# Performance work log

Measured on AMD Instinct MI355X. Metric: run time of the kernel, lower is better.

## Reference

```python
import jax, jax.numpy as jnp
import numpy as np

B, S, E, H, FF = 4, 2048, 1024, 16, 4096
DK = E // H
EPS = 1e-5


def setup_inputs() -> dict:
    key = jax.random.key(0)
    ks = jax.random.split(key, 16)
    sc = 0.02
    return {
        "x": jax.random.normal(ks[0], (B, S, E), jnp.float32),
        "Wq": jax.random.normal(ks[1], (E, E), jnp.float32) * sc,
        "Wk": jax.random.normal(ks[2], (E, E), jnp.float32) * sc,
        "Wv": jax.random.normal(ks[3], (E, E), jnp.float32) * sc,
        "Wo": jax.random.normal(ks[4], (E, E), jnp.float32) * sc,
        "theta": jax.random.normal(ks[5], (DK,), jnp.float32),
        "Wcq": jax.random.normal(ks[6], (E, E), jnp.float32) * sc,
        "ln1_g": jnp.ones((E,), jnp.float32),
        "ln1_b": jnp.zeros((E,), jnp.float32),
        "W1": jax.random.normal(ks[7], (E, FF), jnp.float32) * sc,
        "b1": jnp.zeros((FF,), jnp.float32),
        "W2": jax.random.normal(ks[8], (FF, E), jnp.float32) * sc,
        "b2": jnp.zeros((E,), jnp.float32),
        "ln2_g": jnp.ones((E,), jnp.float32),
        "ln2_b": jnp.zeros((E,), jnp.float32),
    }


def _layernorm(x, g, b):
    mu = jnp.mean(x, axis=-1, keepdims=True)
    var = jnp.mean(jnp.square(x - mu), axis=-1, keepdims=True)
    return (x - mu) * jax.lax.rsqrt(var + EPS) * g + b


def reference(x, Wq, Wk, Wv, Wo, theta, Wcq, ln1_g, ln1_b, W1, b1, W2, b2, ln2_g, ln2_b):
    mix = 0.5
    # classical multi-head attention
    def heads(t):  # [B,S,E] -> [B,H,S,DK]
        return t.reshape(B, S, H, DK).transpose(0, 2, 1, 3)
    q = heads(x @ Wq)
    k = heads(x @ Wk)
    v = heads(x @ Wv)
    scores = jnp.einsum("bhqd,bhkd->bhqk", q, k) / jnp.sqrt(jnp.float32(DK))
    attn = jax.nn.softmax(scores, axis=-1)
    ctx = jnp.einsum("bhqk,bhkd->bhqd", attn, v)
    ctx = ctx.transpose(0, 2, 1, 3).reshape(B, S, E)
    classical = ctx @ Wo
    # quantum heads: RX(x)RX(theta)|0>, <Z> = cos(x + theta), same theta shared per head
    qh = jnp.cos(x.reshape(B, S, H, DK) + theta)  # broadcast over wires
    quantum = qh.reshape(B, S, E) @ Wcq
    attn_out = mix * classical + (1.0 - mix) * quantum
    x1 = _layernorm(x + attn_out, ln1_g, ln1_b)
    ffn = jax.nn.relu(x1 @ W1 + b1) @ W2 + b2
    return _layernorm(x1 + ffn, ln2_g, ln2_b)
```

## Files before the change

kernel.cpp:

```cpp
#include <hip/hip_runtime.h>
#include <hip/hip_bf16.h>

typedef __bf16 bf16_t;
typedef bf16_t bf16x8 __attribute__((ext_vector_type(8)));
typedef bf16_t bf16x4v __attribute__((ext_vector_type(4)));
typedef float f32x4 __attribute__((ext_vector_type(4)));
typedef unsigned u32x4 __attribute__((ext_vector_type(4)));

static constexpr int EE = 1024;
static constexpr int SS = 2048;
static constexpr int DK = 64;
static constexpr float QSCALE = 0.125f * 1.44269504f;

__device__ __forceinline__ void gload_lds16(const void* g, void* l) {
  __builtin_amdgcn_global_load_lds(
      (__attribute__((address_space(1))) void*)g,
      (__attribute__((address_space(3))) void*)l, 16, 0, 0);
}

__device__ __forceinline__ f32x4 mfma16(bf16x8 a, bf16x8 b, f32x4 c) {
  return __builtin_amdgcn_mfma_f32_16x16x32_bf16(a, b, c, 0, 0, 0);
}

template<int OFF>
__device__ __forceinline__ bf16x4v tr8(unsigned va) {
  bf16x4v d;
  asm volatile("ds_read_b64_tr_b16 %0, %1 offset:%c2"
               : "=v"(d) : "v"(va), "i"(OFF));
  return d;
}

__global__ void __launch_bounds__(256) prep_x_kernel(
    const float* __restrict__ x, const float* __restrict__ theta,
    bf16_t* __restrict__ xbf, bf16_t* __restrict__ A2)
{
  const long t = (long)blockIdx.x * 256 + threadIdx.x;
  const long e0 = t * 8;
  const int col = (int)(e0 & (EE - 1));
  const long row = e0 >> 10;
  const float4 v0 = *(const float4*)&x[e0];
  const float4 v1 = *(const float4*)&x[e0 + 4];
  float xs[8] = {v0.x, v0.y, v0.z, v0.w, v1.x, v1.y, v1.z, v1.w};
  const int d0 = col & (DK - 1);
  bf16x8 xb, qb;
#pragma unroll
  for (int j = 0; j < 8; ++j) {
    xb[j] = (bf16_t)xs[j];
    qb[j] = (bf16_t)__cosf(xs[j] + theta[d0 + j]);
  }
  *(bf16x8*)&xbf[e0] = xb;
  *(bf16x8*)&A2[row * 2048 + EE + col] = qb;
}

__global__ void __launch_bounds__(256) transpose_all_kernel(
    const float* __restrict__ Wq, const float* __restrict__ Wk,
    const float* __restrict__ Wv, const float* __restrict__ Wo,
    const float* __restrict__ Wcq, const float* __restrict__ W1,
    const float* __restrict__ W2,
    bf16_t* __restrict__ BtQKV, bf16_t* __restrict__ Bt2,
    bf16_t* __restrict__ BtW1, bf16_t* __restrict__ BtW2)
{
  const int bid = blockIdx.x;
  const float* src; bf16_t* dst; int N; long dstride, dcol0; int bx, by;
  if (bid < 5120) {
    const int seg = bid >> 10, r = bid & 1023;
    bx = r & 31; by = r >> 5; N = 1024;
    if      (seg == 0) { src = Wq;  dst = BtQKV;               dstride = 1024; dcol0 = 0; }
    else if (seg == 1) { src = Wk;  dst = BtQKV + 1024 * 1024; dstride = 1024; dcol0 = 0; }
    else if (seg == 2) { src = Wv;  dst = BtQKV + 2048 * 1024; dstride = 1024; dcol0 = 0; }
    else if (seg == 3) { src = Wo;  dst = Bt2;                 dstride = 2048; dcol0 = 0; }
    else               { src = Wcq; dst = Bt2;                 dstride = 2048; dcol0 = 1024; }
  } else if (bid < 9216) {
    const int r = bid - 5120;
    src = W1; dst = BtW1; N = 4096; dstride = 1024; dcol0 = 0;
    bx = r & 127; by = r >> 7;
  } else {
    const int r = bid - 9216;
    src = W2; dst = BtW2; N = 1024; dstride = 4096; dcol0 = 0;
    bx = r & 31; by = r >> 5;
  }
  __shared__ float tile[32][33];
  const int tx = threadIdx.x, ty = threadIdx.y;
  const long n0 = (long)bx * 32, k0 = (long)by * 32;
#pragma unroll
  for (int j = 0; j < 4; ++j)
    tile[ty + j * 8][tx] = src[(k0 + ty + j * 8) * N + n0 + tx];
  __syncthreads();
#pragma unroll
  for (int j = 0; j < 4; ++j)
    dst[(n0 + ty + j * 8) * dstride + dcol0 + k0 + tx] = (bf16_t)tile[tx][ty + j * 8];
}

template<int MODE>
__global__ void __launch_bounds__(512, 4) gemm128(
    const bf16_t* __restrict__ A, const bf16_t* __restrict__ Bt,
    void* __restrict__ C, int M, int N, int K,
    const float* __restrict__ aux1, const bf16_t* __restrict__ aux2)
{
  __shared__ bf16_t As[3][256 * 32];
  __shared__ bf16_t Bs[3][128 * 32];
  const int tid = threadIdx.x;
  const int lane = tid & 63, wid = tid >> 6;
  const int wr = wid >> 1, wc = wid & 1;
  const int lr = lane & 15, lk = lane >> 4;
  const int gx = gridDim.x;
  const int nwg = gx * gridDim.y;
  const int bid = blockIdx.y * gx + blockIdx.x;
  const int swz = (bid & 7) * (nwg >> 3) + (bid >> 3);
  const long m0 = (long)(swz / gx) * 256;
  const long n0 = (long)(swz % gx) * 128;

  const int rql = lane >> 2;
  const int sl  = lane & 3;
  const int rA0 = wid * 32 + rql, rA1 = wid * 32 + 16 + rql;
  const bf16_t* sA0 = &A [(m0 + rA0) * K + 8 * (sl ^ ((rA0 >> 1) & 3))];
  const bf16_t* sA1 = &A [(m0 + rA1) * K + 8 * (sl ^ ((rA1 >> 1) & 3))];
  const int rB0 = wid * 16 + rql;
  const bf16_t* sB0 = &Bt[(n0 + rB0) * K + 8 * (sl ^ ((rB0 >> 1) & 3))];
  const int loA = wid * 1024;
  const int loB = wid * 512;

  f32x4 acc[4][4] = {};
  const int NKT = K / 32;

  auto stage = [&](int t) {
    const int s = t % 3;
    gload_lds16(sA0 + (long)t * 32, &As[s][loA]);
    gload_lds16(sA1 + (long)t * 32, &As[s][loA + 512]);
    gload_lds16(sB0 + (long)t * 32, &Bs[s][loB]);
  };

  stage(0); stage(1);
  asm volatile("s_waitcnt vmcnt(3)" ::: "memory");
  __builtin_amdgcn_s_barrier();

  for (int t = 0; t < NKT; ++t) {
    const int s = t % 3;
    bf16x8 bfr[4], af1[2], af2[2];
#pragma unroll
    for (int nb = 0; nb < 4; ++nb) {
      const int rw = wc * 64 + nb * 16 + lr;
      bfr[nb] = *(const bf16x8*)&Bs[s][rw * 32 + (lk ^ ((rw >> 1) & 3)) * 8];
    }
#pragma unroll
    for (int mb = 0; mb < 2; ++mb) {
      const int rw = wr * 64 + mb * 16 + lr;
      af1[mb] = *(const bf16x8*)&As[s][rw * 32 + (lk ^ ((rw >> 1) & 3)) * 8];
    }
    __builtin_amdgcn_sched_barrier(0);
#pragma unroll
    for (int mb = 0; mb < 2; ++mb) {
      const int rw = wr * 64 + 32 + mb * 16 + lr;
      af2[mb] = *(const bf16x8*)&As[s][rw * 32 + (lk ^ ((rw >> 1) & 3)) * 8];
    }
    if (t + 2 < NKT) stage(t + 2);
    asm volatile("s_waitcnt lgkmcnt(2)" ::: "memory");
    __builtin_amdgcn_sched_barrier(0);
    __builtin_amdgcn_s_setprio(1);
#pragma unroll
    for (int mb = 0; mb < 2; ++mb)
#pragma unroll
      for (int nb = 0; nb < 4; ++nb)
        acc[mb][nb] = mfma16(af1[mb], bfr[nb], acc[mb][nb]);
    __builtin_amdgcn_s_setprio(0);
    asm volatile("s_waitcnt lgkmcnt(0)" ::: "memory");
    __builtin_amdgcn_sched_barrier(0);
    __builtin_amdgcn_s_setprio(1);
#pragma unroll
    for (int mb = 0; mb < 2; ++mb)
#pragma unroll
      for (int nb = 0; nb < 4; ++nb)
        acc[2 + mb][nb] = mfma16(af2[mb], bfr[nb], acc[2 + mb][nb]);
    __builtin_amdgcn_s_setprio(0);
    if (t + 2 < NKT)      { asm volatile("s_waitcnt vmcnt(3)" ::: "memory"); }
    else if (t + 1 < NKT) { asm volatile("s_waitcnt vmcnt(0)" ::: "memory"); }
    __builtin_amdgcn_s_barrier();
  }

#pragma unroll
  for (int mb = 0; mb < 4; ++mb)
#pragma unroll
    for (int nb = 0; nb < 4; ++nb)
#pragma unroll
      for (int i = 0; i < 4; ++i) {
        const long r = m0 + wr * 64 + mb * 16 + lk * 4 + i;
        const long cc = n0 + wc * 64 + nb * 16 + lr;
        float v = acc[mb][nb][i];
        if constexpr (MODE == 0) {
          if (cc < 1024) v *= QSCALE;
          ((bf16_t*)C)[r * N + cc] = (bf16_t)v;
        } else if constexpr (MODE == 1) {
          ((bf16_t*)C)[r * N + cc] = (bf16_t)(0.5f * v + (float)aux2[r * N + cc]);
        } else if constexpr (MODE == 2) {
          ((bf16_t*)C)[r * N + cc] = (bf16_t)fmaxf(v + aux1[cc], 0.0f);
        } else {
          ((bf16_t*)C)[r * N + cc] = (bf16_t)(v + aux1[cc] + (float)aux2[r * N + cc]);
        }
      }
}

__global__ void __launch_bounds__(256, 2) attn_kernel(
    const bf16_t* __restrict__ QKV, bf16_t* __restrict__ Ctx)
{
  __shared__ bf16_t Ks[2][64 * 64];
  __shared__ bf16_t Vt[2][64 * 64];
  const int tid = threadIdx.x;
  const int lane = tid & 63, w = tid >> 6;
  const int lr = lane & 15, lk = lane >> 4;
  const int bh = blockIdx.x, b = bh >> 4, h = bh & 15;
  const long rowbase = (long)b * SS;
  const int q0 = blockIdx.y * 128;
  const int qcol = h * 64, kcol = EE + h * 64, vcol = 2 * EE + h * 64;
  constexpr int NT = SS / 64;

  bf16x8 qf[2][2];
#pragma unroll
  for (int mb = 0; mb < 2; ++mb)
#pragma unroll
    for (int ks = 0; ks < 2; ++ks)
      qf[mb][ks] = *(const bf16x8*)&QKV[
          (rowbase + q0 + w * 32 + mb * 16 + lr) * 3072 + qcol + ks * 32 + lk * 8];

  const int ksl = ((lane & 7) ^ ((lane >> 3) & 7)) * 8;
  const bf16_t* sK0 = &QKV[(rowbase + (2 * w + 0) * 8 + (lane >> 3)) * 3072 + kcol + ksl];
  const bf16_t* sK1 = &QKV[(rowbase + (2 * w + 1) * 8 + (lane >> 3)) * 3072 + kcol + ksl];
  const int vk = 4 * (lane >> 3) + ((lane >> 1) & 3);
  const int vd = 16 * w + 8 * (lane & 1);
  const bf16_t* sV0 = &QKV[(rowbase + vk) * 3072 + vcol + vd];
  const bf16_t* sV1 = &QKV[(rowbase + 32 + vk) * 3072 + vcol + vd];

  auto stage = [&](int t) {
    const int buf = t & 1;
    const long off = (long)t * 64 * 3072;
    gload_lds16(sK0 + off, &Ks[buf][(2 * w + 0) * 512]);
    gload_lds16(sK1 + off, &Ks[buf][(2 * w + 1) * 512]);
    gload_lds16(sV0 + off, &Vt[buf][(2 * w + 0) * 512]);
    gload_lds16(sV1 + off, &Vt[buf][(2 * w + 1) * 512]);
  };

  const unsigned vtr_base =
      (unsigned)(uintptr_t)(__attribute__((address_space(3))) void*)&Vt[0][0]
      + 2u * (unsigned)(lr + lk * 64);

  f32x4 oacc[2][4] = {};
  float lsum[2] = {0.0f, 0.0f};

  stage(0);

  for (int t = 0; t < NT; ++t) {
    const int buf = t & 1;
    __syncthreads();
    if (t + 1 < NT) stage(t + 1);

    bf16x8 kf[4][2];
#pragma unroll
    for (int nb = 0; nb < 4; ++nb)
#pragma unroll
      for (int ks = 0; ks < 2; ++ks)
        kf[nb][ks] = *(const bf16x8*)&Ks[buf][
            (nb * 16 + lr) * 64 + ((ks * 4 + lk) ^ (lr & 7)) * 8];
    __builtin_amdgcn_sched_barrier(0);

    const unsigned va = vtr_base + (unsigned)buf * 8192u;
    bf16x4v vlo[4][2], vhi[4][2];
    vlo[0][0] = tr8<   0>(va);  vhi[0][0] = tr8< 512>(va);
    vlo[0][1] = tr8<1024>(va);  vhi[0][1] = tr8<1536>(va);
    vlo[1][0] = tr8<2048>(va);  vhi[1][0] = tr8<2560>(va);
    vlo[1][1] = tr8<3072>(va);  vhi[1][1] = tr8<3584>(va);
    vlo[2][0] = tr8<4096>(va);  vhi[2][0] = tr8<4608>(va);
    vlo[2][1] = tr8<5120>(va);  vhi[2][1] = tr8<5632>(va);
    vlo[3][0] = tr8<6144>(va);  vhi[3][0] = tr8<6656>(va);
    vlo[3][1] = tr8<7168>(va);  vhi[3][1] = tr8<7680>(va);

    asm volatile("s_waitcnt lgkmcnt(15)" ::: "memory");
    __builtin_amdgcn_sched_barrier(0);

    f32x4 sacc[2][4] = {};
    __builtin_amdgcn_s_setprio(1);
#pragma unroll
    for (int mb = 0; mb < 2; ++mb)
#pragma unroll
      for (int nb = 0; nb < 4; ++nb)
#pragma unroll
        for (int ks = 0; ks < 2; ++ks)
          sacc[mb][nb] = mfma16(kf[nb][ks], qf[mb][ks], sacc[mb][nb]);
    __builtin_amdgcn_s_setprio(0);

    bf16x8 pfm[2][2];
#pragma unroll
    for (int mb = 0; mb < 2; ++mb) {
      float psum = 0.0f;
      u32x4 pk[2];
#pragma unroll
      for (int nb = 0; nb < 4; ++nb)
#pragma unroll
        for (int p = 0; p < 2; ++p) {
          const float a = __builtin_amdgcn_exp2f(sacc[mb][nb][2 * p]);
          const float bb = __builtin_amdgcn_exp2f(sacc[mb][nb][2 * p + 1]);
          psum += a + bb;
          unsigned pr;
          asm("v_cvt_pk_bf16_f32 %0, %1, %2" : "=v"(pr) : "v"(a), "v"(bb));
          pk[nb >> 1][(nb & 1) * 2 + p] = pr;
        }
      lsum[mb] += psum;
      pfm[mb][0] = __builtin_bit_cast(bf16x8, pk[0]);
      pfm[mb][1] = __builtin_bit_cast(bf16x8, pk[1]);
    }

    asm volatile("s_waitcnt lgkmcnt(0)" ::: "memory");
    __builtin_amdgcn_sched_barrier(0);
    bf16x8 vf[4][2];
#pragma unroll
    for (int nb = 0; nb < 4; ++nb)
#pragma unroll
      for (int ks = 0; ks < 2; ++ks)
        vf[nb][ks] = __builtin_shufflevector(
            vlo[nb][ks], vhi[nb][ks], 0, 1, 2, 3, 4, 5, 6, 7);
    __builtin_amdgcn_s_setprio(1);
#pragma unroll
    for (int mb = 0; mb < 2; ++mb)
#pragma unroll
      for (int nb = 0; nb < 4; ++nb)
#pragma unroll
        for (int ks = 0; ks < 2; ++ks)
          oacc[mb][nb] = mfma16(pfm[mb][ks], vf[nb][ks], oacc[mb][nb]);
    __builtin_amdgcn_s_setprio(0);
  }

#pragma unroll
  for (int mb = 0; mb < 2; ++mb) {
    float l = lsum[mb];
    l += __shfl_xor(l, 16);
    l += __shfl_xor(l, 32);
    float li[4];
#pragma unroll
    for (int i = 0; i < 4; ++i) li[i] = 1.0f / __shfl(l, lk * 4 + i);
#pragma unroll
    for (int nb = 0; nb < 4; ++nb)
#pragma unroll
      for (int i = 0; i < 4; ++i) {
        const long r = rowbase + q0 + w * 32 + mb * 16 + lk * 4 + i;
        Ctx[r * 2048 + h * 64 + nb * 16 + lr] = (bf16_t)(oacc[mb][nb][i] * li[i]);
      }
  }
}

__device__ __forceinline__ void ln_reduce4(const float4& v, int tid,
                                           float& mu, float& rs) {
  float s = v.x + v.y + v.z + v.w;
  float ss = v.x * v.x + v.y * v.y + v.z * v.z + v.w * v.w;
#pragma unroll
  for (int off = 1; off < 64; off <<= 1) {
    s += __shfl_xor(s, off);
    ss += __shfl_xor(ss, off);
  }
  __shared__ float wsum[4], wsq[4];
  if ((tid & 63) == 0) { wsum[tid >> 6] = s; wsq[tid >> 6] = ss; }
  __syncthreads();
  s = wsum[0] + wsum[1] + wsum[2] + wsum[3];
  ss = wsq[0] + wsq[1] + wsq[2] + wsq[3];
  mu = s * (1.0f / EE);
  rs = rsqrtf(ss * (1.0f / EE) - mu * mu + 1e-5f);
}

__global__ void __launch_bounds__(256) ln_bf16_kernel(
    const bf16_t* __restrict__ pre, const float* __restrict__ g,
    const float* __restrict__ bt, bf16_t* __restrict__ out)
{
  const int r = blockIdx.x, tid = threadIdx.x;
  const long base = (long)r * EE + tid * 4;
  const bf16x4v pv = *(const bf16x4v*)&pre[base];
  float4 v = make_float4((float)pv[0], (float)pv[1], (float)pv[2], (float)pv[3]);
  float mu, rs;
  ln_reduce4(v, tid, mu, rs);
  const float4 gv = *(const float4*)&g[tid * 4];
  const float4 bv = *(const float4*)&bt[tid * 4];
  bf16x4v o;
  o[0] = (bf16_t)((v.x - mu) * rs * gv.x + bv.x);
  o[1] = (bf16_t)((v.y - mu) * rs * gv.y + bv.y);
  o[2] = (bf16_t)((v.z - mu) * rs * gv.z + bv.z);
  o[3] = (bf16_t)((v.w - mu) * rs * gv.w + bv.w);
  *(bf16x4v*)&out[base] = o;
}

__global__ void __launch_bounds__(256) ln_f32_kernel(
    const bf16_t* __restrict__ pre, const float* __restrict__ g,
    const float* __restrict__ bt, float* __restrict__ out)
{
  const int r = blockIdx.x, tid = threadIdx.x;
  const long base = (long)r * EE + tid * 4;
  const bf16x4v pv = *(const bf16x4v*)&pre[base];
  float4 v = make_float4((float)pv[0], (float)pv[1], (float)pv[2], (float)pv[3]);
  float mu, rs;
  ln_reduce4(v, tid, mu, rs);
  const float4 gv = *(const float4*)&g[tid * 4];
  const float4 bv = *(const float4*)&bt[tid * 4];
  float4 o;
  o.x = (v.x - mu) * rs * gv.x + bv.x;
  o.y = (v.y - mu) * rs * gv.y + bv.y;
  o.z = (v.z - mu) * rs * gv.z + bv.z;
  o.w = (v.w - mu) * rs * gv.w + bv.w;
  *(float4*)&out[base] = o;
}

extern "C" void kernel_launch(void* const* d_in, const int* in_sizes, int n_in,
                              void* d_out, int out_size, void* d_ws, size_t ws_size,
                              hipStream_t stream)
{
  (void)in_sizes; (void)n_in; (void)out_size; (void)ws_size;
  const float* x     = (const float*)d_in[0];
  const float* Wq    = (const float*)d_in[1];
  const float* Wk    = (const float*)d_in[2];
  const float* Wv    = (const float*)d_in[3];
  const float* Wo    = (const float*)d_in[4];
  const float* theta = (const float*)d_in[5];
  const float* Wcq   = (const float*)d_in[6];
  const float* ln1g  = (const float*)d_in[7];
  const float* ln1b  = (const float*)d_in[8];
  const float* W1    = (const float*)d_in[9];
  const float* b1    = (const float*)d_in[10];
  const float* W2    = (const float*)d_in[11];
  const float* b2    = (const float*)d_in[12];
  const float* ln2g  = (const float*)d_in[13];
  const float* ln2b  = (const float*)d_in[14];

  char* ws = (char*)d_ws;
  const size_t MB = 1ull << 20;
  bf16_t* xbf     = (bf16_t*)(ws + 0);
  bf16_t* QKV     = (bf16_t*)(ws + 16 * MB);
  bf16_t* preLN1  = (bf16_t*)(ws + 16 * MB);
  bf16_t* A2      = (bf16_t*)(ws + 64 * MB);
  bf16_t* preLN2  = (bf16_t*)(ws + 64 * MB);
  bf16_t* H1      = (bf16_t*)(ws + 96 * MB);
  bf16_t* BtQKV   = (bf16_t*)(ws + 160 * MB);
  bf16_t* Bt2     = (bf16_t*)(ws + 166 * MB);
  bf16_t* BtW1    = (bf16_t*)(ws + 170 * MB);
  bf16_t* BtW2    = (bf16_t*)(ws + 178 * MB);

  prep_x_kernel<<<4096, 256, 0, stream>>>(x, theta, xbf, A2);
  transpose_all_kernel<<<13312, dim3(32, 8), 0, stream>>>(
      Wq, Wk, Wv, Wo, Wcq, W1, W2, BtQKV, Bt2, BtW1, BtW2);

  gemm128<0><<<dim3(24, 32), 512, 0, stream>>>(xbf, BtQKV, QKV, 8192, 3072, 1024, nullptr, nullptr);
  attn_kernel<<<dim3(64, 16), 256, 0, stream>>>(QKV, A2);
  gemm128<1><<<dim3(8, 32), 512, 0, stream>>>(A2, Bt2, preLN1, 8192, 1024, 2048, nullptr, xbf);
  ln_bf16_kernel<<<8192, 256, 0, stream>>>(preLN1, ln1g, ln1b, xbf);
  gemm128<2><<<dim3(32, 32), 512, 0, stream>>>(xbf, BtW1, H1, 8192, 4096, 1024, b1, nullptr);
  gemm128<3><<<dim3(8, 32), 512, 0, stream>>>(H1, BtW2, preLN2, 8192, 1024, 4096, b2, xbf);
  ln_f32_kernel<<<8192, 256, 0, stream>>>(preLN2, ln2g, ln2b, (float*)d_out);
}
```

Measured before the change: 407.9 us.

## Add 256x256 eight-wave ping-pong GEMM for QKV and FFN1 projections

Introduces a new GEMM kernel with 256x256 output tiles, K-step 64, double-buffered LDS loaded via global_load_lds with an XOR swizzle, and a phased schedule that interleaves fragment reads, next-tile prefetch and MFMA blocks between barriers with priority raising. The QKV and W1 projections switch to this kernel, halving the grid and raising arithmetic intensity per tile. The cost is 128 KB of LDS per block, so occupancy is limited to one or two blocks per CU. There are also many barriers per K-step, and wave quantization at the smaller grid sizes is a risk.

```diff
diff --git a/kernel.cpp b/kernel.cpp
--- a/kernel.cpp
+++ b/kernel.cpp
@@ -91,6 +91,104 @@
     dst[(n0 + ty + j * 8) * dstride + dcol0 + k0 + tx] = (bf16_t)tile[tx][ty + j * 8];
 }
 
+#define GP_BAR __builtin_amdgcn_s_barrier()
+#define GP_LG0 asm volatile("s_waitcnt lgkmcnt(0)" ::: "memory")
+#define GP_VM0 asm volatile("s_waitcnt vmcnt(0)" ::: "memory")
+#define GP_SCB __builtin_amdgcn_sched_barrier(0)
+#define GP_P1 __builtin_amdgcn_s_setprio(1)
+#define GP_P0 __builtin_amdgcn_s_setprio(0)
+#define GP_SA(bb, h, tt) do { \
+    gload_lds16(bA + (long)((h) * 128) * K + (long)(tt) * 64, \
+                &AsF[((bb) * 2 + (h)) * 8192 + wid * 512]); \
+    gload_lds16(bA + (long)((h) * 128 + 64) * K + (long)(tt) * 64, \
+                &AsF[((bb) * 2 + (h)) * 8192 + 4096 + wid * 512]); } while (0)
+#define GP_SB(bb, h, tt) do { \
+    gload_lds16(bB + (long)((h) * 128) * K + (long)(tt) * 64, \
+                &BsF[((bb) * 2 + (h)) * 8192 + wid * 512]); \
+    gload_lds16(bB + (long)((h) * 128 + 64) * K + (long)(tt) * 64, \
+                &BsF[((bb) * 2 + (h)) * 8192 + 4096 + wid * 512]); } while (0)
+#define GP_RA(bb, mh) do { \
+    _Pragma("unroll") for (int mb2 = 0; mb2 < 4; ++mb2) \
+    _Pragma("unroll") for (int ks = 0; ks < 2; ++ks) { \
+      const int r_ = (mh) * 64 + mb2 * 16 + lr; \
+      fa[mh][mb2][ks] = *(const bf16x8*)&AsF[ \
+          ((bb) * 2 + wr) * 8192 + r_ * 64 + (((ks << 2) | lk) ^ (r_ & 7)) * 8]; } } while (0)
+#define GP_RB(bb, nh) do { \
+    _Pragma("unroll") for (int nb2 = 0; nb2 < 2; ++nb2) \
+    _Pragma("unroll") for (int ks = 0; ks < 2; ++ks) { \
+      const int rw_ = wc * 64 + (nh) * 32 + nb2 * 16 + lr; \
+      fb[nh][nb2][ks] = *(const bf16x8*)&BsF[ \
+          ((bb) * 2 + (wc >> 1)) * 8192 + (rw_ & 127) * 64 + (((ks << 2) | lk) ^ (rw_ & 7)) * 8]; } } while (0)
+#define GP_MM(mh, nh) do { \
+    _Pragma("unroll") for (int mb2 = 0; mb2 < 4; ++mb2) \
+    _Pragma("unroll") for (int nb2 = 0; nb2 < 2; ++nb2) \
+    _Pragma("unroll") for (int ks = 0; ks < 2; ++ks) \
+      acc[(mh) * 4 + mb2][(nh) * 2 + nb2] = \
+          mfma16(fa[mh][mb2][ks], fb[nh][nb2][ks], acc[(mh) * 4 + mb2][(nh) * 2 + nb2]); } while (0)
+
+template<int MODE>
+__global__ void __launch_bounds__(512, 2) gemm8p(
+    const bf16_t* __restrict__ A, const bf16_t* __restrict__ Bt,
+    void* __restrict__ C, int M, int N, int K, const float* __restrict__ aux1)
+{
+  __shared__ bf16_t AsF[32768];
+  __shared__ bf16_t BsF[32768];
+  const int tid = threadIdx.x;
+  const int lane = tid & 63, wid = tid >> 6;
+  const int wr = wid >> 2, wc = wid & 3;
+  const int lr = lane & 15, lk = lane >> 4;
+  const int gx = gridDim.x;
+  const int nwg = gx * gridDim.y;
+  const int bid = blockIdx.y * gx + blockIdx.x;
+  const int swz = (bid & 7) * (nwg >> 3) + (bid >> 3);
+  const long m0 = (long)(swz / gx) * 256;
+  const long n0 = (long)(swz % gx) * 256;
+
+  const int strow = tid >> 3, stslot = tid & 7;
+  const int scol = 8 * (stslot ^ (strow & 7));
+  const bf16_t* bA = &A [(m0 + strow) * K + scol];
+  const bf16_t* bB = &Bt[(n0 + strow) * K + scol];
+
+  f32x4 acc[8][4] = {};
+  bf16x8 fa[2][4][2], fb[2][2][2];
+  const int NKT = K / 64;
+
+  GP_SA(0, 0, 0); GP_SA(0, 1, 0);
+  GP_SB(0, 0, 0); GP_SB(0, 1, 0);
+  GP_VM0; GP_BAR;
+
+  for (int t = 0; t < NKT; ++t) {
+    const int b = t & 1, nb = b ^ 1;
+    GP_RA(b, 0); GP_RB(b, 0);
+    if (t + 1 < NKT) { GP_SA(nb, 0, t + 1); GP_SA(nb, 1, t + 1); }
+    GP_BAR; GP_LG0; GP_SCB; GP_P1; GP_MM(0, 0); GP_P0; GP_BAR;
+    GP_RB(b, 1);
+    if (t + 1 < NKT) { GP_SB(nb, 0, t + 1); GP_SB(nb, 1, t + 1); }
+    GP_BAR; GP_LG0; GP_SCB; GP_P1; GP_MM(0, 1); GP_P0; GP_BAR;
+    GP_RA(b, 1);
+    GP_BAR; GP_LG0; GP_SCB; GP_P1; GP_MM(1, 0); GP_P0; GP_BAR;
+    GP_VM0; GP_BAR;
+    GP_P1; GP_MM(1, 1); GP_P0; GP_BAR;
+  }
+
+#pragma unroll
+  for (int mb = 0; mb < 8; ++mb)
+#pragma unroll
+    for (int nb = 0; nb < 4; ++nb)
+#pragma unroll
+      for (int i = 0; i < 4; ++i) {
+        const long r = m0 + wr * 128 + (mb >> 2) * 64 + (mb & 3) * 16 + lk * 4 + i;
+        const long cc = n0 + wc * 64 + (nb >> 1) * 32 + (nb & 1) * 16 + lr;
+        float v = acc[mb][nb][i];
+        if constexpr (MODE == 0) {
+          if (cc < 1024) v *= QSCALE;
+          ((bf16_t*)C)[r * N + cc] = (bf16_t)v;
+        } else {
+          ((bf16_t*)C)[r * N + cc] = (bf16_t)fmaxf(v + aux1[cc], 0.0f);
+        }
+      }
+}
+
 template<int MODE>
 __global__ void __launch_bounds__(512, 4) gemm128(
     const bf16_t* __restrict__ A, const bf16_t* __restrict__ Bt,
@@ -186,13 +284,8 @@
         const long r = m0 + wr * 64 + mb * 16 + lk * 4 + i;
         const long cc = n0 + wc * 64 + nb * 16 + lr;
         float v = acc[mb][nb][i];
-        if constexpr (MODE == 0) {
-          if (cc < 1024) v *= QSCALE;
-          ((bf16_t*)C)[r * N + cc] = (bf16_t)v;
-        } else if constexpr (MODE == 1) {
+        if constexpr (MODE == 1) {
           ((bf16_t*)C)[r * N + cc] = (bf16_t)(0.5f * v + (float)aux2[r * N + cc]);
-        } else if constexpr (MODE == 2) {
-          ((bf16_t*)C)[r * N + cc] = (bf16_t)fmaxf(v + aux1[cc], 0.0f);
         } else {
           ((bf16_t*)C)[r * N + cc] = (bf16_t)(v + aux1[cc] + (float)aux2[r * N + cc]);
         }
@@ -441,11 +534,11 @@
   transpose_all_kernel<<<13312, dim3(32, 8), 0, stream>>>(
       Wq, Wk, Wv, Wo, Wcq, W1, W2, BtQKV, Bt2, BtW1, BtW2);
 
-  gemm128<0><<<dim3(24, 32), 512, 0, stream>>>(xbf, BtQKV, QKV, 8192, 3072, 1024, nullptr, nullptr);
+  gemm8p<0><<<dim3(12, 32), 512, 0, stream>>>(xbf, BtQKV, QKV, 8192, 3072, 1024, nullptr);
   attn_kernel<<<dim3(64, 16), 256, 0, stream>>>(QKV, A2);
   gemm128<1><<<dim3(8, 32), 512, 0, stream>>>(A2, Bt2, preLN1, 8192, 1024, 2048, nullptr, xbf);
   ln_bf16_kernel<<<8192, 256, 0, stream>>>(preLN1, ln1g, ln1b, xbf);
-  gemm128<2><<<dim3(32, 32), 512, 0, stream>>>(xbf, BtW1, H1, 8192, 4096, 1024, b1, nullptr);
+  gemm8p<2><<<dim3(16, 32), 512, 0, stream>>>(xbf, BtW1, H1, 8192, 4096, 1024, b1);
   gemm128<3><<<dim3(8, 32), 512, 0, stream>>>(H1, BtW2, preLN2, 8192, 1024, 4096, b2, xbf);
   ln_f32_kernel<<<8192, 256, 0, stream>>>(preLN2, ln2g, ln2b, (float*)d_out);
 }
```

Result: no change. 400.5 us (median of 2 runs) (-1.8%).

## Replace GEMM with 8-phase ping-pong pipelined kernel and 256x256 tiles for FFN1

Applied to the files above, without the earlier changes.

Rewrites the bf16 GEMM as a templated kernel with K-step 64, double-buffered LDS and an 8-wave schedule. Each iteration is split into four MFMA quadrants, and the global-to-LDS loads for the next tile are interleaved between barriers. An XOR swizzle over 8 slots is used, and the FFN up-projection now uses 256x256 tiles to improve reuse. The goal is better overlap of memory traffic with MFMA and fewer LDS bank conflicts. In exchange, LDS use per block is higher, occupancy drops (launch bounds go from 4 to 2 blocks), and each iteration carries more barriers.

```diff
diff --git a/kernel.cpp b/kernel.cpp
--- a/kernel.cpp
+++ b/kernel.cpp
@@ -91,100 +91,139 @@
     dst[(n0 + ty + j * 8) * dstride + dcol0 + k0 + tx] = (bf16_t)tile[tx][ty + j * 8];
 }
 
-template<int MODE>
-__global__ void __launch_bounds__(512, 4) gemm128(
+#define GP_BAR __builtin_amdgcn_s_barrier()
+#define GP_LG0 asm volatile("s_waitcnt lgkmcnt(0)" ::: "memory")
+#define GP_VM0 asm volatile("s_waitcnt vmcnt(0)" ::: "memory")
+#define GP_SCB __builtin_amdgcn_sched_barrier(0)
+#define GP_P1 __builtin_amdgcn_s_setprio(1)
+#define GP_P0 __builtin_amdgcn_s_setprio(0)
+
+template<int MODE, int TN>
+__global__ void __launch_bounds__(512, 2) gemm8p(
     const bf16_t* __restrict__ A, const bf16_t* __restrict__ Bt,
     void* __restrict__ C, int M, int N, int K,
     const float* __restrict__ aux1, const bf16_t* __restrict__ aux2)
 {
-  __shared__ bf16_t As[3][256 * 32];
-  __shared__ bf16_t Bs[3][128 * 32];
+  constexpr int MBQ = (TN == 256) ? 4 : 2;
+  __shared__ bf16_t AsF[32768];
+  __shared__ bf16_t BsF[(TN == 256) ? 32768 : 16384];
   const int tid = threadIdx.x;
   const int lane = tid & 63, wid = tid >> 6;
-  const int wr = wid >> 1, wc = wid & 1;
+  const int wr = (TN == 256) ? (wid >> 2) : (wid >> 1);
+  const int wc = (TN == 256) ? (wid & 3) : (wid & 1);
   const int lr = lane & 15, lk = lane >> 4;
   const int gx = gridDim.x;
   const int nwg = gx * gridDim.y;
   const int bid = blockIdx.y * gx + blockIdx.x;
   const int swz = (bid & 7) * (nwg >> 3) + (bid >> 3);
   const long m0 = (long)(swz / gx) * 256;
-  const long n0 = (long)(swz % gx) * 128;
-
-  const int rql = lane >> 2;
-  const int sl  = lane & 3;
-  const int rA0 = wid * 32 + rql, rA1 = wid * 32 + 16 + rql;
-  const bf16_t* sA0 = &A [(m0 + rA0) * K + 8 * (sl ^ ((rA0 >> 1) & 3))];
-  const bf16_t* sA1 = &A [(m0 + rA1) * K + 8 * (sl ^ ((rA1 >> 1) & 3))];
-  const int rB0 = wid * 16 + rql;
-  const bf16_t* sB0 = &Bt[(n0 + rB0) * K + 8 * (sl ^ ((rB0 >> 1) & 3))];
-  const int loA = wid * 1024;
-  const int loB = wid * 512;
-
-  f32x4 acc[4][4] = {};
-  const int NKT = K / 32;
-
-  auto stage = [&](int t) {
-    const int s = t % 3;
-    gload_lds16(sA0 + (long)t * 32, &As[s][loA]);
-    gload_lds16(sA1 + (long)t * 32, &As[s][loA + 512]);
-    gload_lds16(sB0 + (long)t * 32, &Bs[s][loB]);
-  };
-
-  stage(0); stage(1);
-  asm volatile("s_waitcnt vmcnt(3)" ::: "memory");
-  __builtin_amdgcn_s_barrier();
+  const long n0 = (long)(swz % gx) * TN;
+
+  const int strow = tid >> 3, stslot = tid & 7;
+  const int scol = 8 * (stslot ^ (strow & 7));
+  const bf16_t* bA = &A [(m0 + strow) * K + scol];
+  const bf16_t* bB = &Bt[(n0 + strow) * K + scol];
+
+  f32x4 acc[MBQ * 2][4] = {};
+  bf16x8 fa[2][MBQ][2], fb[2][2][2];
+  const int NKT = K / 64;
+
+  auto stA = [&](int bb, int h, int tt) {
+    gload_lds16(bA + (long)(h * 128) * K + (long)tt * 64,
+                &AsF[(bb * 2 + h) * 8192 + wid * 512]);
+    gload_lds16(bA + (long)(h * 128 + 64) * K + (long)tt * 64,
+                &AsF[(bb * 2 + h) * 8192 + 4096 + wid * 512]);
+  };
+  auto stBh = [&](int bb, int h, int tt) {
+    gload_lds16(bB + (long)(h * 128) * K + (long)tt * 64,
+                &BsF[(bb * 2 + h) * 8192 + wid * 512]);
+    gload_lds16(bB + (long)(h * 128 + 64) * K + (long)tt * 64,
+                &BsF[(bb * 2 + h) * 8192 + 4096 + wid * 512]);
+  };
+  auto stB128 = [&](int bb, int tt) {
+    gload_lds16(bB + (long)tt * 64, &BsF[(bb * 2 + 0) * 4096 + wid * 512]);
+    gload_lds16(bB + (long)64 * K + (long)tt * 64,
+                &BsF[(bb * 2 + 1) * 4096 + wid * 512]);
+  };
+  auto rdA = [&](int bb, int mh) {
+#pragma unroll
+    for (int m2 = 0; m2 < MBQ; ++m2)
+#pragma unroll
+      for (int ks = 0; ks < 2; ++ks) {
+        int r_, hf;
+        if constexpr (TN == 256) { r_ = mh * 64 + m2 * 16 + lr; hf = wr; }
+        else { r_ = (wr & 1) * 64 + mh * 32 + m2 * 16 + lr; hf = wr >> 1; }
+        fa[mh][m2][ks] = *(const bf16x8*)&AsF[
+            (bb * 2 + hf) * 8192 + r_ * 64 + (((ks << 2) | lk) ^ (r_ & 7)) * 8];
+      }
+  };
+  auto rdB = [&](int bb, int nh) {
+#pragma unroll
+    for (int n2 = 0; n2 < 2; ++n2)
+#pragma unroll
+      for (int ks = 0; ks < 2; ++ks) {
+        if constexpr (TN == 256) {
+          const int rw_ = wc * 64 + nh * 32 + n2 * 16 + lr;
+          fb[nh][n2][ks] = *(const bf16x8*)&BsF[
+              (bb * 2 + (wc >> 1)) * 8192 + (rw_ & 127) * 64 +
+              (((ks << 2) | lk) ^ (rw_ & 7)) * 8];
+        } else {
+          const int rB = nh * 32 + n2 * 16 + lr;
+          fb[nh][n2][ks] = *(const bf16x8*)&BsF[
+              (bb * 2 + wc) * 4096 + rB * 64 +
+              (((ks << 2) | lk) ^ (rB & 7)) * 8];
+        }
+      }
+  };
+  auto mm = [&](int mh, int nh) {
+#pragma unroll
+    for (int m2 = 0; m2 < MBQ; ++m2)
+#pragma unroll
+      for (int n2 = 0; n2 < 2; ++n2)
+#pragma unroll
+        for (int ks = 0; ks < 2; ++ks)
+          acc[mh * MBQ + m2][nh * 2 + n2] =
+              mfma16(fa[mh][m2][ks], fb[nh][n2][ks], acc[mh * MBQ + m2][nh * 2 + n2]);
+  };
+
+  stA(0, 0, 0); stA(0, 1, 0);
+  if constexpr (TN == 256) { stBh(0, 0, 0); stBh(0, 1, 0); }
+  else                     { stB128(0, 0); }
+  GP_VM0; GP_BAR;
 
   for (int t = 0; t < NKT; ++t) {
-    const int s = t % 3;
-    bf16x8 bfr[4], af1[2], af2[2];
-#pragma unroll
-    for (int nb = 0; nb < 4; ++nb) {
-      const int rw = wc * 64 + nb * 16 + lr;
-      bfr[nb] = *(const bf16x8*)&Bs[s][rw * 32 + (lk ^ ((rw >> 1) & 3)) * 8];
+    const int b = t & 1, nbuf = b ^ 1;
+    rdA(b, 0); rdB(b, 0);
+    if (t + 1 < NKT) {
+      if constexpr (TN == 256) { stA(nbuf, 0, t + 1); stA(nbuf, 1, t + 1); }
+      else                     { stA(nbuf, 0, t + 1); }
     }
-#pragma unroll
-    for (int mb = 0; mb < 2; ++mb) {
-      const int rw = wr * 64 + mb * 16 + lr;
-      af1[mb] = *(const bf16x8*)&As[s][rw * 32 + (lk ^ ((rw >> 1) & 3)) * 8];
+    GP_BAR; GP_LG0; GP_SCB; GP_P1; mm(0, 0); GP_P0; GP_BAR;
+    rdB(b, 1);
+    if (t + 1 < NKT) {
+      if constexpr (TN == 256) { stBh(nbuf, 0, t + 1); stBh(nbuf, 1, t + 1); }
+      else                     { stA(nbuf, 1, t + 1); }
     }
-    __builtin_amdgcn_sched_barrier(0);
-#pragma unroll
-    for (int mb = 0; mb < 2; ++mb) {
-      const int rw = wr * 64 + 32 + mb * 16 + lr;
-      af2[mb] = *(const bf16x8*)&As[s][rw * 32 + (lk ^ ((rw >> 1) & 3)) * 8];
-    }
-    if (t + 2 < NKT) stage(t + 2);
-    asm volatile("s_waitcnt lgkmcnt(2)" ::: "memory");
-    __builtin_amdgcn_sched_barrier(0);
-    __builtin_amdgcn_s_setprio(1);
-#pragma unroll
-    for (int mb = 0; mb < 2; ++mb)
-#pragma unroll
-      for (int nb = 0; nb < 4; ++nb)
-        acc[mb][nb] = mfma16(af1[mb], bfr[nb], acc[mb][nb]);
-    __builtin_amdgcn_s_setprio(0);
-    asm volatile("s_waitcnt lgkmcnt(0)" ::: "memory");
-    __builtin_amdgcn_sched_barrier(0);
-    __builtin_amdgcn_s_setprio(1);
-#pragma unroll
-    for (int mb = 0; mb < 2; ++mb)
-#pragma unroll
-      for (int nb = 0; nb < 4; ++nb)
-        acc[2 + mb][nb] = mfma16(af2[mb], bfr[nb], acc[2 + mb][nb]);
-    __builtin_amdgcn_s_setprio(0);
-    if (t + 2 < NKT)      { asm volatile("s_waitcnt vmcnt(3)" ::: "memory"); }
-    else if (t + 1 < NKT) { asm volatile("s_waitcnt vmcnt(0)" ::: "memory"); }
-    __builtin_amdgcn_s_barrier();
-  }
-
-#pragma unroll
-  for (int mb = 0; mb < 4; ++mb)
+    GP_BAR; GP_LG0; GP_SCB; GP_P1; mm(0, 1); GP_P0; GP_BAR;
+    rdA(b, 1);
+    if (t + 1 < NKT) { if constexpr (TN == 128) stB128(nbuf, t + 1); }
+    GP_BAR; GP_LG0; GP_SCB; GP_P1; mm(1, 0); GP_P0; GP_BAR;
+    GP_VM0; GP_BAR;
+    GP_P1; mm(1, 1); GP_P0; GP_BAR;
+  }
+
+#pragma unroll
+  for (int mb = 0; mb < MBQ * 2; ++mb)
 #pragma unroll
     for (int nb = 0; nb < 4; ++nb)
 #pragma unroll
       for (int i = 0; i < 4; ++i) {
-        const long r = m0 + wr * 64 + mb * 16 + lk * 4 + i;
-        const long cc = n0 + wc * 64 + nb * 16 + lr;
+        long r;
+        if constexpr (TN == 256)
+          r = m0 + wr * 128 + (mb >> 2) * 64 + (mb & 3) * 16 + lk * 4 + i;
+        else
+          r = m0 + wr * 64 + (mb >> 1) * 32 + (mb & 1) * 16 + lk * 4 + i;
+        const long cc = n0 + wc * 64 + (nb >> 1) * 32 + (nb & 1) * 16 + lr;
         float v = acc[mb][nb][i];
         if constexpr (MODE == 0) {
           if (cc < 1024) v *= QSCALE;
@@ -441,11 +480,11 @@
   transpose_all_kernel<<<13312, dim3(32, 8), 0, stream>>>(
       Wq, Wk, Wv, Wo, Wcq, W1, W2, BtQKV, Bt2, BtW1, BtW2);
 
-  gemm128<0><<<dim3(24, 32), 512, 0, stream>>>(xbf, BtQKV, QKV, 8192, 3072, 1024, nullptr, nullptr);
+  gemm8p<0, 128><<<dim3(24, 32), 512, 0, stream>>>(xbf, BtQKV, QKV, 8192, 3072, 1024, nullptr, nullptr);
   attn_kernel<<<dim3(64, 16), 256, 0, stream>>>(QKV, A2);
-  gemm128<1><<<dim3(8, 32), 512, 0, stream>>>(A2, Bt2, preLN1, 8192, 1024, 2048, nullptr, xbf);
+  gemm8p<1, 128><<<dim3(8, 32), 512, 0, stream>>>(A2, Bt2, preLN1, 8192, 1024, 2048, nullptr, xbf);
   ln_bf16_kernel<<<8192, 256, 0, stream>>>(preLN1, ln1g, ln1b, xbf);
-  gemm128<2><<<dim3(32, 32), 512, 0, stream>>>(xbf, BtW1, H1, 8192, 4096, 1024, b1, nullptr);
-  gemm128<3><<<dim3(8, 32), 512, 0, stream>>>(H1, BtW2, preLN2, 8192, 1024, 4096, b2, xbf);
+  gemm8p<2, 256><<<dim3(16, 32), 512, 0, stream>>>(xbf, BtW1, H1, 8192, 4096, 1024, b1, nullptr);
+  gemm8p<3, 128><<<dim3(8, 32), 512, 0, stream>>>(H1, BtW2, preLN2, 8192, 1024, 4096, b2, xbf);
   ln_f32_kernel<<<8192, 256, 0, stream>>>(preLN2, ln2g, ln2b, (float*)d_out);
 }
```

New measurement: 425.9 us. 1.04x slower.
